# Kernel tuning notes

Hardware: AMD Instinct MI355X
Metric: run time of the kernel (lower is better)

## Reference

```python
import jax, jax.numpy as jnp
import numpy as np

K = 8192      # codebook_dim
D = 256       # embedding_dim
BETA = 0.25
DECAY = 0.99
EPS = 1e-05


def setup_inputs() -> dict:
    key = jax.random.key(0)
    k1, k2, k3, k4 = jax.random.split(key, 4)
    lim = 1.0 / K
    return {
        "z": jax.random.normal(k1, (8, D, 32, 32), dtype=jnp.float32),
        "embedding": jax.random.uniform(k2, (K, D), minval=-lim, maxval=lim, dtype=jnp.float32),
        "cluster_size": jax.random.uniform(k3, (K,), dtype=jnp.float32),
        "ema_w": jax.random.uniform(k4, (K, D), minval=-lim, maxval=lim, dtype=jnp.float32),
    }


def reference(z, embedding, cluster_size, ema_w):
    # z: [B, C, H, W] -> [B, H, W, C]
    zp = jnp.transpose(z, (0, 2, 3, 1))
    zf = zp.reshape(-1, D)                                  # [N, D]
    # squared L2 distance to each code: ||z||^2 + ||e||^2 - 2 z.e
    d = (jnp.sum(zf * zf, axis=1, keepdims=True)
         + jnp.sum(embedding * embedding, axis=1)
         - 2.0 * jnp.einsum("nd,kd->nk", zf, embedding))    # [N, K]
    idx = jnp.argmin(d, axis=1)                             # [N]
    z_q = embedding[idx].reshape(zp.shape)                  # [B, H, W, C]

    # EMA update (training branch), expressed with segment sums instead of
    # materializing the one-hot [N, K] matrix.
    counts = jax.ops.segment_sum(jnp.ones_like(idx, dtype=zf.dtype), idx, num_segments=K)
    new_cs = cluster_size * DECAY + (1.0 - DECAY) * counts
    n = jnp.sum(new_cs)
    new_cs = (new_cs + EPS) / (n + K * EPS) * n
    dw = jax.ops.segment_sum(zf, idx, num_segments=K)       # encodings.T @ zf
    new_ema_w = ema_w * DECAY + (1.0 - DECAY) * dw
    new_embedding = new_ema_w / new_cs[:, None]

    sg = jax.lax.stop_gradient
    loss = jnp.mean((sg(z_q) - zp) ** 2) + BETA * jnp.mean((z_q - sg(zp)) ** 2)
    # straight-through estimator, back to NCHW
    z_q_out = jnp.transpose(zp + sg(z_q - zp), (0, 3, 1, 2))
    return z_q_out, loss, idx, new_cs, new_ema_w, new_embedding
```

## Files before the change

### kernel.cpp

```cpp
#include <hip/hip_runtime.h>

#define CHW 262144
#define HWD 1024

typedef _Float16 v8h __attribute__((ext_vector_type(8)));
typedef _Float16 v4h __attribute__((ext_vector_type(4)));
typedef float    v4f __attribute__((ext_vector_type(4)));

static const unsigned OFF_ASQ  = 0;
static const unsigned OFF_BSQ  = 8192;
static const unsigned OFF_CNT  = 16384;
static const unsigned OFF_HEAD = 24576;
static const unsigned OFF_NXT  = 32768;
static const unsigned OFF_SCAL = 40960;
static const unsigned OFF_AH   = 40968;
static const unsigned OFF_AM   = 1089544;
static const unsigned OFF_BH   = 2138120;
static const unsigned OFF_BM   = 3186696;

#define GLL(g, l) __builtin_amdgcn_global_load_lds( \
    (const __attribute__((address_space(1))) void*)(g), \
    (__attribute__((address_space(3))) void*)(l), 16, 0, 0)

__global__ __launch_bounds__(256) void k_prep(const float* __restrict__ z,
        const float* __restrict__ emb, float* __restrict__ asq, float* __restrict__ bsq,
        _Float16* __restrict__ Bh, _Float16* __restrict__ Bm,
        _Float16* __restrict__ Ah, _Float16* __restrict__ Am,
        float* __restrict__ zerobase) {
    int bx = blockIdx.x;
    int t = threadIdx.x;
    if (bx < 32) {
        int n = bx * 256 + t;
        const float* p = z + (size_t)(n >> 10) * CHW + (n & 1023);
        float s = 0.f;
        #pragma unroll 8
        for (int c = 0; c < 256; ++c) { float v = p[(size_t)c << 10]; s = fmaf(v, v, s); }
        asq[n] = s;
    } else if (bx < 2080) {
        int w = (bx - 32) * 4 + (t >> 6);
        int lane = t & 63;
        float4 v = *(const float4*)(emb + (size_t)w * 256 + lane * 4);
        float s = v.x * v.x;
        s = fmaf(v.y, v.y, s); s = fmaf(v.z, v.z, s); s = fmaf(v.w, v.w, s);
        #pragma unroll
        for (int m = 1; m < 64; m <<= 1) s += __shfl_xor(s, m, 64);
        if (lane == 0) bsq[w] = s;
        float e0 = v.x * 8192.0f, e1 = v.y * 8192.0f, e2 = v.z * 8192.0f, e3 = v.w * 8192.0f;
        _Float16 h0 = (_Float16)e0, h1 = (_Float16)e1, h2 = (_Float16)e2, h3 = (_Float16)e3;
        v4h hv = {h0, h1, h2, h3};
        v4h mv = {(_Float16)((e0 - (float)h0) * 2048.0f),
                  (_Float16)((e1 - (float)h1) * 2048.0f),
                  (_Float16)((e2 - (float)h2) * 2048.0f),
                  (_Float16)((e3 - (float)h3) * 2048.0f)};
        *(v4h*)(Bh + (size_t)w * 256 + lane * 4) = hv;
        *(v4h*)(Bm + (size_t)w * 256 + lane * 4) = mv;
    } else if (bx < 2592) {
        __shared__ float s[64][65];
        int blk = bx - 2080;
        int hw0 = (blk & 15) * 64;
        int c0  = ((blk >> 4) & 3) * 64;
        int b   = blk >> 6;
        #pragma unroll
        for (int ii = 0; ii < 16; ++ii) {
            int e = t + ii * 256;
            int c = e >> 6, x = e & 63;
            s[c][x] = z[(size_t)b * CHW + (size_t)(c0 + c) * HWD + hw0 + x];
        }
        __syncthreads();
        int n = t & 63, cseg = (t >> 6) * 16;
        _Float16 hbuf[16], mbuf[16];
        #pragma unroll
        for (int j = 0; j < 16; ++j) {
            float v = s[cseg + j][n];
            _Float16 h = (_Float16)v;
            float r = v - (float)h;
            hbuf[j] = h;
            mbuf[j] = (_Float16)(r * 2048.0f);
        }
        size_t off = ((size_t)b * 1024 + hw0 + n) * 256 + c0 + cseg;
        *(v8h*)(Ah + off)     = *(v8h*)(hbuf);
        *(v8h*)(Ah + off + 8) = *(v8h*)(hbuf + 8);
        *(v8h*)(Am + off)     = *(v8h*)(mbuf);
        *(v8h*)(Am + off + 8) = *(v8h*)(mbuf + 8);
    } else {
        int idx = (bx - 2592) * 1024 + t * 4;
        *(float4*)(zerobase + idx) = (float4){0.f, 0.f, 0.f, 0.f};
        if (bx == 2592 && t == 0)
            *(float4*)(zerobase + 24576) = (float4){0.f, 0.f, 0.f, 0.f};
    }
}

__global__ __launch_bounds__(256, 2) void k_main(
        const _Float16* __restrict__ Ah, const _Float16* __restrict__ Am,
        const _Float16* __restrict__ Bh, const _Float16* __restrict__ Bm,
        const float* __restrict__ asq, const float* __restrict__ bsq,
        unsigned* __restrict__ pdk) {
    __shared__ _Float16 lds[32768];
    const int kt = blockIdx.x, nt = blockIdx.y;
    const int n0 = nt * 128, k0 = kt * 128;
    const int t = threadIdx.x;
    const int lane = t & 63, w = t >> 6;
    const int wrow = w >> 1, wcol = w & 1;
    const int lm = lane & 15, quad = lane >> 4;

    v4f acc1[4][4], acc2[4][4];
    #pragma unroll
    for (int i = 0; i < 4; ++i)
        #pragma unroll
        for (int j = 0; j < 4; ++j) { acc1[i][j] = (v4f){0.f,0.f,0.f,0.f}; acc2[i][j] = (v4f){0.f,0.f,0.f,0.f}; }

    const int row0 = t >> 2;
    const int c40 = (t & 3) ^ ((row0 >> 1) & 3);
    const char* gA  = (const char*)Ah + (size_t)(n0 + row0) * 512 + c40 * 16;
    const char* gAm = (const char*)Am + (size_t)(n0 + row0) * 512 + c40 * 16;
    const char* gB  = (const char*)Bh + (size_t)(k0 + row0) * 512 + c40 * 16;
    const char* gBm = (const char*)Bm + (size_t)(k0 + row0) * 512 + c40 * 16;

    int sa[4], sb[4];
    #pragma unroll
    for (int i = 0; i < 4; ++i) {
        int mr = wrow * 64 + i * 16 + lm;
        sa[i] = mr * 32 + ((quad ^ ((mr >> 1) & 3)) * 8);
    }
    #pragma unroll
    for (int j = 0; j < 4; ++j) {
        int nr = wcol * 64 + j * 16 + lm;
        sb[j] = nr * 32 + ((quad ^ ((nr >> 1) & 3)) * 8);
    }

    auto stage = [&](int cb, int buf) {
        const size_t co = (size_t)cb * 64;
        _Float16* l = lds + buf * 16384 + t * 8;
        GLL(gA + co,           l);
        GLL(gA + co + 32768,   l + 2048);
        GLL(gAm + co,          l + 4096);
        GLL(gAm + co + 32768,  l + 6144);
        GLL(gB + co,           l + 8192);
        GLL(gB + co + 32768,   l + 10240);
        GLL(gBm + co,          l + 12288);
        GLL(gBm + co + 32768,  l + 14336);
    };

#define MFMA16(A, B, C) __builtin_amdgcn_mfma_f32_16x16x32_f16(A, B, C, 0, 0, 0)
#define PROD(I, J, FA, FAM, FB, FBM) do { \
        acc1[I][J] = MFMA16(FA,  FB,  acc1[I][J]); \
        acc2[I][J] = MFMA16(FA,  FBM, acc2[I][J]); \
        acc2[I][J] = MFMA16(FAM, FB,  acc2[I][J]); \
    } while (0)

    stage(0, 0);
    for (int cb = 0; cb < 8; ++cb) {
        asm volatile("s_waitcnt vmcnt(0)" ::: "memory");
        __builtin_amdgcn_s_barrier();
        __builtin_amdgcn_sched_barrier(0);
        if (cb < 7) stage(cb + 1, (cb + 1) & 1);
        const _Float16* L = lds + (cb & 1) * 16384;

        v8h fa0  = *(const v8h*)(L + sa[0]);
        v8h fa1  = *(const v8h*)(L + sa[1]);
        v8h fam0 = *(const v8h*)(L + 4096 + sa[0]);
        v8h fam1 = *(const v8h*)(L + 4096 + sa[1]);
        v8h fb0  = *(const v8h*)(L + 8192 + sb[0]);
        v8h fb1  = *(const v8h*)(L + 8192 + sb[1]);
        v8h fbm0 = *(const v8h*)(L + 12288 + sb[0]);
        v8h fbm1 = *(const v8h*)(L + 12288 + sb[1]);
        __builtin_amdgcn_s_setprio(1);
        PROD(0, 0, fa0, fam0, fb0, fbm0);
        PROD(0, 1, fa0, fam0, fb1, fbm1);
        PROD(1, 0, fa1, fam1, fb0, fbm0);
        PROD(1, 1, fa1, fam1, fb1, fbm1);
        __builtin_amdgcn_s_setprio(0);
        __builtin_amdgcn_sched_barrier(0);

        v8h fa2  = *(const v8h*)(L + sa[2]);
        v8h fa3  = *(const v8h*)(L + sa[3]);
        v8h fam2 = *(const v8h*)(L + 4096 + sa[2]);
        v8h fam3 = *(const v8h*)(L + 4096 + sa[3]);
        __builtin_amdgcn_s_setprio(1);
        PROD(2, 0, fa2, fam2, fb0, fbm0);
        PROD(2, 1, fa2, fam2, fb1, fbm1);
        PROD(3, 0, fa3, fam3, fb0, fbm0);
        PROD(3, 1, fa3, fam3, fb1, fbm1);
        __builtin_amdgcn_s_setprio(0);
        __builtin_amdgcn_sched_barrier(0);

        v8h fb2  = *(const v8h*)(L + 8192 + sb[2]);
        v8h fb3  = *(const v8h*)(L + 8192 + sb[3]);
        v8h fbm2 = *(const v8h*)(L + 12288 + sb[2]);
        v8h fbm3 = *(const v8h*)(L + 12288 + sb[3]);
        __builtin_amdgcn_s_setprio(1);
        PROD(0, 2, fa0, fam0, fb2, fbm2);
        PROD(0, 3, fa0, fam0, fb3, fbm3);
        PROD(1, 2, fa1, fam1, fb2, fbm2);
        PROD(1, 3, fa1, fam1, fb3, fbm3);
        __builtin_amdgcn_s_setprio(0);
        __builtin_amdgcn_sched_barrier(0);

        __builtin_amdgcn_s_setprio(1);
        PROD(2, 2, fa2, fam2, fb2, fbm2);
        PROD(2, 3, fa2, fam2, fb3, fbm3);
        PROD(3, 2, fa3, fam3, fb2, fbm2);
        PROD(3, 3, fa3, fam3, fb3, fbm3);
        __builtin_amdgcn_s_setprio(0);
        __builtin_amdgcn_sched_barrier(0);
    }
#undef PROD
#undef MFMA16

    float bvv[4];
    #pragma unroll
    for (int j = 0; j < 4; ++j) bvv[j] = bsq[k0 + wcol * 64 + j * 16 + lm];
    __syncthreads();
    unsigned* lrow = (unsigned*)lds;
    #pragma unroll
    for (int i = 0; i < 4; ++i) {
        #pragma unroll
        for (int r = 0; r < 4; ++r) {
            int mm = wrow * 64 + i * 16 + quad * 4 + r;
            float av_ = asq[n0 + mm];
            unsigned best = 0xFFFFFFFFu;
            #pragma unroll
            for (int j = 0; j < 4; ++j) {
                float S = fmaf(acc2[i][j][r], 4.8828125e-4f, acc1[i][j][r]) * 1.220703125e-4f;
                float dd = (av_ + bvv[j]) - 2.0f * S;
                float gv = dd - av_;
                int mi = (int)(gv * 65536.0f) + 32768;
                int col = k0 + wcol * 64 + j * 16 + lm;
                unsigned key = ((unsigned)mi << 13) | (unsigned)col;
                best = key < best ? key : best;
            }
            #pragma unroll
            for (int xm = 1; xm < 16; xm <<= 1) {
                unsigned o = __shfl_xor(best, xm, 64);
                best = o < best ? o : best;
            }
            if (lm == 0) lrow[wcol * 128 + mm] = best;
        }
    }
    __syncthreads();
    if (t < 256) pdk[(((size_t)nt * 128 + kt * 2) << 7) + t] = lrow[t];
}

__global__ __launch_bounds__(256) void k_zqr(const unsigned* __restrict__ pdk,
        const float* __restrict__ z, const float* __restrict__ emb, const float* __restrict__ cs,
        float* __restrict__ out_idx, int* __restrict__ cnt,
        int* __restrict__ head, int* __restrict__ nxt,
        float* __restrict__ out_zq, float* __restrict__ scal) {
    const int bx = blockIdx.x, by = blockIdx.y;
    const int n0 = bx * 64, c00 = by * 64;
    const int lane = threadIdx.x & 63, g = threadIdx.x >> 6;
    const int nt = bx >> 1, mb = (bx & 1) * 64;

    unsigned mn = 0xFFFFFFFFu;
    const unsigned* base = pdk + (((size_t)nt * 128 + g * 32) << 7) + mb + lane;
    #pragma unroll 8
    for (int jj = 0; jj < 32; ++jj) {
        unsigned key = base[jj << 7];
        mn = key < mn ? key : mn;
    }
    __shared__ unsigned part[4][64];
    part[g][lane] = mn;
    __syncthreads();
    unsigned k0v = part[0][lane], k1v = part[1][lane];
    unsigned k2v = part[2][lane], k3v = part[3][lane];
    unsigned f01 = k0v < k1v ? k0v : k1v;
    unsigned f23 = k2v < k3v ? k2v : k3v;
    unsigned fkey = f01 < f23 ? f01 : f23;
    int idxn = (int)(fkey & 8191u);
    int n = n0 + lane;

    if (by == 0) {
        if (g == 0) {
            out_idx[n] = (float)idxn;
            atomicAdd(cnt + idxn, 1);
            int old = atomicExch(head + idxn, n + 1);
            nxt[n] = old;
        } else if (g == 1) {
            float cv = cs[n];
            #pragma unroll
            for (int m = 1; m < 64; m <<= 1) cv += __shfl_xor(cv, m, 64);
            if (lane == 0) atomicAdd(scal + 1, cv);
        }
    }

    int b = n >> 10, hw = n & 1023;
    const float* zr = z + (size_t)b * CHW + hw;
    const float* er = emb + (size_t)idxn * 256;
    float* oz = out_zq + (size_t)b * CHW + hw;
    float ls = 0.f;
    #pragma unroll
    for (int q = 0; q < 4; ++q) {
        int c = c00 + g * 16 + q * 4;
        float4 e4 = *(const float4*)(er + c);
        float ev[4] = {e4.x, e4.y, e4.z, e4.w};
        #pragma unroll
        for (int r = 0; r < 4; ++r) {
            float zp = zr[(size_t)(c + r) << 10];
            float dif = ev[r] - zp;
            oz[(size_t)(c + r) << 10] = zp + dif;
            ls = fmaf(dif, dif, ls);
        }
    }
    #pragma unroll
    for (int m = 1; m < 64; m <<= 1) ls += __shfl_xor(ls, m, 64);
    __shared__ float red[4];
    if (lane == 0) red[g] = ls;
    __syncthreads();
    if (threadIdx.x == 0) atomicAdd(scal, red[0] + red[1] + red[2] + red[3]);
}

__global__ __launch_bounds__(256) void k_fin(const float* __restrict__ cs, const float* __restrict__ ema,
        const int* __restrict__ head, const int* __restrict__ nxt,
        const _Float16* __restrict__ Ah, const _Float16* __restrict__ Am,
        const float* __restrict__ scal, const int* __restrict__ cnt,
        float* __restrict__ out_ncs, float* __restrict__ out_ema,
        float* __restrict__ out_emb, float* __restrict__ out_loss) {
    int k = blockIdx.x * 4 + (threadIdx.x >> 6);
    int lane = threadIdx.x & 63;
    float4 dwv = {0.f, 0.f, 0.f, 0.f};
    int cur = head[k];
    while (cur) {
        int n = cur - 1;
        v4h hh = *(const v4h*)(Ah + (size_t)n * 256 + lane * 4);
        v4h mm = *(const v4h*)(Am + (size_t)n * 256 + lane * 4);
        dwv.x += fmaf((float)mm[0], 4.8828125e-4f, (float)hh[0]);
        dwv.y += fmaf((float)mm[1], 4.8828125e-4f, (float)hh[1]);
        dwv.z += fmaf((float)mm[2], 4.8828125e-4f, (float)hh[2]);
        dwv.w += fmaf((float)mm[3], 4.8828125e-4f, (float)hh[3]);
        cur = nxt[n];
    }
    const float C1 = (float)(1.0 - 0.99);
    const float KEPS = (float)(8192 * 1e-5);
    float ncs0v = cs[k] * 0.99f + C1 * (float)cnt[k];
    float nsum = 0.99f * scal[1] + C1 * 8192.0f;
    float ncs = (ncs0v + 1e-5f) / (nsum + KEPS) * nsum;
    if (lane == 0) out_ncs[k] = ncs;
    size_t base = (size_t)k * 256 + lane * 4;
    float4 e4 = *(const float4*)(ema + base);
    float r0 = e4.x * 0.99f + C1 * dwv.x;
    float r1 = e4.y * 0.99f + C1 * dwv.y;
    float r2 = e4.z * 0.99f + C1 * dwv.z;
    float r3 = e4.w * 0.99f + C1 * dwv.w;
    out_ema[base + 0] = r0; out_ema[base + 1] = r1; out_ema[base + 2] = r2; out_ema[base + 3] = r3;
    out_emb[base + 0] = r0 / ncs; out_emb[base + 1] = r1 / ncs;
    out_emb[base + 2] = r2 / ncs; out_emb[base + 3] = r3 / ncs;
    if (blockIdx.x == 0 && threadIdx.x == 0) {
        float m = scal[0] * (1.0f / 2097152.0f);
        out_loss[0] = m + 0.25f * m;
    }
}

extern "C" void kernel_launch(void* const* d_in, const int* in_sizes, int n_in,
                              void* d_out, int out_size, void* d_ws, size_t ws_size,
                              hipStream_t stream) {
    const float* z   = (const float*)d_in[0];
    const float* emb = (const float*)d_in[1];
    const float* cs  = (const float*)d_in[2];
    const float* ema = (const float*)d_in[3];
    float* out = (float*)d_out;
    float* wsf = (float*)d_ws;

    float* asq  = wsf + OFF_ASQ;
    float* bsq  = wsf + OFF_BSQ;
    int*   cnt  = (int*)(wsf + OFF_CNT);
    int*   head = (int*)(wsf + OFF_HEAD);
    int*   nxt  = (int*)(wsf + OFF_NXT);
    float* scal = wsf + OFF_SCAL;
    _Float16* Ah = (_Float16*)(wsf + OFF_AH);
    _Float16* Am = (_Float16*)(wsf + OFF_AM);
    _Float16* Bh = (_Float16*)(wsf + OFF_BH);
    _Float16* Bm = (_Float16*)(wsf + OFF_BM);

    float* out_zq   = out;
    float* out_loss = out + 2097152;
    float* out_idx  = out + 2097153;
    float* out_ncs  = out + 2105345;
    float* out_ema  = out + 2113537;
    float* out_emb  = out + 4210689;

    unsigned* pdk = (unsigned*)(out + 2113540);

    k_prep<<<2608, 256, 0, stream>>>(z, emb, asq, bsq, Bh, Bm, Ah, Am, wsf + OFF_CNT);
    k_main<<<dim3(64, 64), 256, 0, stream>>>(Ah, Am, Bh, Bm, asq, bsq, pdk);
    k_zqr<<<dim3(128, 4), 256, 0, stream>>>(pdk, z, emb, cs, out_idx, cnt, head, nxt, out_zq, scal);
    k_fin<<<2048, 256, 0, stream>>>(cs, ema, head, nxt, Ah, Am, scal, cnt, out_ncs, out_ema, out_emb, out_loss);
}
```

Before: 247.1 us.

## Enlarge k_main tile to 256x128 with 512 threads and XCD-aware block swizzle

The distance GEMM kernel now uses 512-thread blocks, each covering 256 rows of z by 128 codes, launched as a 1D grid. Block IDs are remapped so that blocks on the same XCD work on a compact rectangle of tiles, which improves L2 reuse. The A tile now sits in a single LDS buffer that is refilled mid-iteration behind an extra barrier, while B stays double-buffered, and the per-row argmin key writes are reindexed to the new tile shape. This raises A/B reuse per block and cuts global traffic, at the cost of an extra barrier per k-step, higher register pressure at 512 threads, and a less overlapped A load.

```diff
diff --git a/kernel.cpp b/kernel.cpp
--- a/kernel.cpp
+++ b/kernel.cpp
@@ -90,14 +90,19 @@
     }
 }
 
-__global__ __launch_bounds__(256, 2) void k_main(
+__global__ __launch_bounds__(512, 2) void k_main(
         const _Float16* __restrict__ Ah, const _Float16* __restrict__ Am,
         const _Float16* __restrict__ Bh, const _Float16* __restrict__ Bm,
         const float* __restrict__ asq, const float* __restrict__ bsq,
         unsigned* __restrict__ pdk) {
     __shared__ _Float16 lds[32768];
-    const int kt = blockIdx.x, nt = blockIdx.y;
-    const int n0 = nt * 128, k0 = kt * 128;
+    const int bid = blockIdx.x;
+    const int xcd = bid & 7, s = bid >> 3;
+    const int rect = s >> 5, rr = s & 31;
+    const int rg = xcd * 8 + rect;
+    const int nt = (rg & 7) * 4 + (rr >> 3);
+    const int kt = (rg >> 3) * 8 + (rr & 7);
+    const int n0 = nt * 256, k0 = kt * 128;
     const int t = threadIdx.x;
     const int lane = t & 63, w = t >> 6;
     const int wrow = w >> 1, wcol = w & 1;
@@ -128,17 +133,19 @@
         sb[j] = nr * 32 + ((quad ^ ((nr >> 1) & 3)) * 8);
     }
 
-    auto stage = [&](int cb, int buf) {
+    auto stageA = [&](int cb) {
         const size_t co = (size_t)cb * 64;
-        _Float16* l = lds + buf * 16384 + t * 8;
+        _Float16* l = lds + t * 8;
         GLL(gA + co,           l);
-        GLL(gA + co + 32768,   l + 2048);
-        GLL(gAm + co,          l + 4096);
-        GLL(gAm + co + 32768,  l + 6144);
-        GLL(gB + co,           l + 8192);
-        GLL(gB + co + 32768,   l + 10240);
-        GLL(gBm + co,          l + 12288);
-        GLL(gBm + co + 32768,  l + 14336);
+        GLL(gA + co + 65536,   l + 4096);
+        GLL(gAm + co,          l + 8192);
+        GLL(gAm + co + 65536,  l + 12288);
+    };
+    auto stageB = [&](int cb, int buf) {
+        const size_t co = (size_t)cb * 64;
+        _Float16* l = lds + 16384 + buf * 8192 + t * 8;
+        GLL(gB + co,  l);
+        GLL(gBm + co, l + 4096);
     };
 
 #define MFMA16(A, B, C) __builtin_amdgcn_mfma_f32_16x16x32_f16(A, B, C, 0, 0, 0)
@@ -148,35 +155,33 @@
         acc2[I][J] = MFMA16(FAM, FB,  acc2[I][J]); \
     } while (0)
 
-    stage(0, 0);
+    stageA(0);
+    stageB(0, 0);
     for (int cb = 0; cb < 8; ++cb) {
         asm volatile("s_waitcnt vmcnt(0)" ::: "memory");
         __builtin_amdgcn_s_barrier();
         __builtin_amdgcn_sched_barrier(0);
-        if (cb < 7) stage(cb + 1, (cb + 1) & 1);
-        const _Float16* L = lds + (cb & 1) * 16384;
-
-        v8h fa0  = *(const v8h*)(L + sa[0]);
-        v8h fa1  = *(const v8h*)(L + sa[1]);
-        v8h fam0 = *(const v8h*)(L + 4096 + sa[0]);
-        v8h fam1 = *(const v8h*)(L + 4096 + sa[1]);
-        v8h fb0  = *(const v8h*)(L + 8192 + sb[0]);
-        v8h fb1  = *(const v8h*)(L + 8192 + sb[1]);
-        v8h fbm0 = *(const v8h*)(L + 12288 + sb[0]);
-        v8h fbm1 = *(const v8h*)(L + 12288 + sb[1]);
+        if (cb < 7) stageB(cb + 1, (cb + 1) & 1);
+        const _Float16* LB = lds + 16384 + (cb & 1) * 8192;
+
+        v8h fa0  = *(const v8h*)(lds + sa[0]);
+        v8h fa1  = *(const v8h*)(lds + sa[1]);
+        v8h fa2  = *(const v8h*)(lds + sa[2]);
+        v8h fa3  = *(const v8h*)(lds + sa[3]);
+        v8h fam0 = *(const v8h*)(lds + 8192 + sa[0]);
+        v8h fam1 = *(const v8h*)(lds + 8192 + sa[1]);
+        v8h fam2 = *(const v8h*)(lds + 8192 + sa[2]);
+        v8h fam3 = *(const v8h*)(lds + 8192 + sa[3]);
+        v8h fb0  = *(const v8h*)(LB + sb[0]);
+        v8h fb1  = *(const v8h*)(LB + sb[1]);
+        v8h fbm0 = *(const v8h*)(LB + 4096 + sb[0]);
+        v8h fbm1 = *(const v8h*)(LB + 4096 + sb[1]);
+
         __builtin_amdgcn_s_setprio(1);
         PROD(0, 0, fa0, fam0, fb0, fbm0);
         PROD(0, 1, fa0, fam0, fb1, fbm1);
         PROD(1, 0, fa1, fam1, fb0, fbm0);
         PROD(1, 1, fa1, fam1, fb1, fbm1);
-        __builtin_amdgcn_s_setprio(0);
-        __builtin_amdgcn_sched_barrier(0);
-
-        v8h fa2  = *(const v8h*)(L + sa[2]);
-        v8h fa3  = *(const v8h*)(L + sa[3]);
-        v8h fam2 = *(const v8h*)(L + 4096 + sa[2]);
-        v8h fam3 = *(const v8h*)(L + 4096 + sa[3]);
-        __builtin_amdgcn_s_setprio(1);
         PROD(2, 0, fa2, fam2, fb0, fbm0);
         PROD(2, 1, fa2, fam2, fb1, fbm1);
         PROD(3, 0, fa3, fam3, fb0, fbm0);
@@ -184,19 +189,21 @@
         __builtin_amdgcn_s_setprio(0);
         __builtin_amdgcn_sched_barrier(0);
 
-        v8h fb2  = *(const v8h*)(L + 8192 + sb[2]);
-        v8h fb3  = *(const v8h*)(L + 8192 + sb[3]);
-        v8h fbm2 = *(const v8h*)(L + 12288 + sb[2]);
-        v8h fbm3 = *(const v8h*)(L + 12288 + sb[3]);
+        asm volatile("s_waitcnt lgkmcnt(0)" ::: "memory");
+        __builtin_amdgcn_s_barrier();
+        __builtin_amdgcn_sched_barrier(0);
+        if (cb < 7) stageA(cb + 1);
+
+        v8h fb2  = *(const v8h*)(LB + sb[2]);
+        v8h fb3  = *(const v8h*)(LB + sb[3]);
+        v8h fbm2 = *(const v8h*)(LB + 4096 + sb[2]);
+        v8h fbm3 = *(const v8h*)(LB + 4096 + sb[3]);
+
         __builtin_amdgcn_s_setprio(1);
         PROD(0, 2, fa0, fam0, fb2, fbm2);
         PROD(0, 3, fa0, fam0, fb3, fbm3);
         PROD(1, 2, fa1, fam1, fb2, fbm2);
         PROD(1, 3, fa1, fam1, fb3, fbm3);
-        __builtin_amdgcn_s_setprio(0);
-        __builtin_amdgcn_sched_barrier(0);
-
-        __builtin_amdgcn_s_setprio(1);
         PROD(2, 2, fa2, fam2, fb2, fbm2);
         PROD(2, 3, fa2, fam2, fb3, fbm3);
         PROD(3, 2, fa3, fam3, fb2, fbm2);
@@ -234,11 +241,15 @@
                 unsigned o = __shfl_xor(best, xm, 64);
                 best = o < best ? o : best;
             }
-            if (lm == 0) lrow[wcol * 128 + mm] = best;
+            if (lm == 0) lrow[wcol * 256 + mm] = best;
         }
     }
     __syncthreads();
-    if (t < 256) pdk[(((size_t)nt * 128 + kt * 2) << 7) + t] = lrow[t];
+    {
+        int mm2 = t & 255, half = t >> 8;
+        pdk[((size_t)(nt * 2 + (mm2 >> 7)) * 128 + kt * 2 + half) * 128 + (mm2 & 127)]
+            = lrow[half * 256 + mm2];
+    }
 }
 
 __global__ __launch_bounds__(256) void k_zqr(const unsigned* __restrict__ pdk,
@@ -381,7 +392,7 @@
     unsigned* pdk = (unsigned*)(out + 2113540);
 
     k_prep<<<2608, 256, 0, stream>>>(z, emb, asq, bsq, Bh, Bm, Ah, Am, wsf + OFF_CNT);
-    k_main<<<dim3(64, 64), 256, 0, stream>>>(Ah, Am, Bh, Bm, asq, bsq, pdk);
+    k_main<<<2048, 512, 0, stream>>>(Ah, Am, Bh, Bm, asq, bsq, pdk);
     k_zqr<<<dim3(128, 4), 256, 0, stream>>>(pdk, z, emb, cs, out_idx, cnt, head, nxt, out_zq, scal);
     k_fin<<<2048, 256, 0, stream>>>(cs, ema, head, nxt, Ah, Am, scal, cnt, out_ncs, out_ema, out_emb, out_loss);
 }
```

Result: no change. 245.4 us (-0.7%).
